# Kernel optimization log

Hardware: AMD Instinct MI355X
Metric: run time of the kernel (lower is better)

Reference implementation:

```python
import jax, jax.numpy as jnp
import numpy as np

THRESH = 0.95
SCALE = 20.0
KERNEL = 8  # feature_hw // proto_grid_size = 64 // 8
EPS = 1e-4


def _avg_pool(x, k):
    # x: [b, c, h, w] -> [b, c, h//k, w//k], non-overlapping k x k mean (AvgPool2d(k))
    b, c, h, w = x.shape
    return x.reshape(b, c, h // k, k, w // k, k).mean(axis=(3, 5))


def _safe_norm(x, eps=EPS):
    # L2-normalize along axis 1, clamping the norm at eps (matches safe_norm)
    n = jnp.sqrt(jnp.sum(x * x, axis=1, keepdims=True))
    return x / jnp.maximum(n, eps)


def setup_inputs() -> dict:
    key = jax.random.key(0)
    k1, k2, k3 = jax.random.split(key, 3)
    qry = jax.random.normal(k1, (32, 256, 64, 64), dtype=jnp.float32)
    sup_x = jax.random.normal(k2, (4, 256, 64, 64), dtype=jnp.float32)
    # binary support mask so that (sup_y > 0.95) selects the ones and pooled
    # occupancy exceeds 0.5 for ~half the grid cells -> valid prototypes exist
    sup_y = jax.random.randint(k3, (4, 1, 64, 64), 0, 2).astype(jnp.float32)
    return {"qry": qry, "sup_x": sup_x, "sup_y": sup_y}


def reference(qry, sup_x, sup_y):
    # ---- normalize query features (gridconv mode) ----
    qn = _safe_norm(qry)                                  # [B, C, H, W]

    # ---- prototype extraction (gridconv) ----
    mask_bin = (sup_y > THRESH).astype(qry.dtype)         # [bs, 1, H, W]
    feat_pooled = _avg_pool(sup_x, KERNEL)                # [bs, C, G, G]
    mask_pooled = _avg_pool(mask_bin, KERNEL)             # [bs, 1, G, G]
    valid = (mask_pooled[:, 0] > 0.5).reshape(-1)         # [P] with P = bs*G*G

    C = feat_pooled.shape[1]
    # gather all pooled locations in (image, hi, wi) order, mask out invalid ones
    protos = jnp.transpose(feat_pooled, (0, 2, 3, 1)).reshape(-1, C)  # [P, C]
    protos_n = _safe_norm(protos)                         # [P, C]

    # ---- prediction: conv2d with 1x1 prototype kernels == channel contraction ----
    dists = jnp.einsum('bchw,pc->bphw', qn, protos_n) * SCALE  # [B, P, H, W]
    vmask = valid[None, :, None, None]
    logits = jnp.where(vmask, dists, -jnp.inf)
    w = jax.nn.softmax(logits, axis=1)                    # invalid protos get 0 weight
    pred = jnp.sum(w * jnp.where(vmask, dists, 0.0), axis=1, keepdims=True)  # [B,1,H,W]

    debug_assign = jnp.argmax(logits, axis=1).astype(dists.dtype)  # [B, H, W]
    proto_grid = mask_bin                                 # (sup_y > thresh).float()
    return (pred, debug_assign, proto_grid)
```

## Files before the change

kernel.cpp:

```cpp
#include <hip/hip_runtime.h>
#include <math.h>

constexpr int BQ = 32;
constexpr int C  = 256;
constexpr int HW = 4096;
constexpr int W  = 64;
constexpr int P  = 256;
constexpr float THRESH = 0.95f;
constexpr float SCALE  = 20.0f;
constexpr float EPSF   = 1e-4f;
constexpr double EPSD  = 1e-4;
constexpr float GAP_THRESH = 2e-3f;
constexpr int MAXSUS = 65536;

constexpr int OUT_ASSIGN = BQ * HW;
constexpr int OUT_GRID   = 2 * BQ * HW;

typedef __attribute__((ext_vector_type(8))) short short8;
typedef __attribute__((ext_vector_type(4))) float floatx4;

static __device__ __forceinline__ unsigned short f2bf(float x) {
    unsigned u = __float_as_uint(x);
    u += 0x7FFFu + ((u >> 16) & 1u);
    return (unsigned short)(u >> 16);
}
static __device__ __forceinline__ float bf2f(unsigned short h) {
    return __uint_as_float(((unsigned)h) << 16);
}

#define FRAGOFF(tile, ks, h, lane) (((((tile) * 8 + (ks)) * 2 + (h)) * 64 + (lane)) * 8)

static __device__ __forceinline__ void gl_lds16(const unsigned short* gp, unsigned short* lp) {
    __builtin_amdgcn_global_load_lds(
        (const __attribute__((address_space(1))) unsigned int*)gp,
        (__attribute__((address_space(3))) unsigned int*)lp, 16, 0, 0);
}

__global__ __launch_bounds__(256)
void prep_kernel(const float* __restrict__ sup_x, const float* __restrict__ sup_y,
                 float* __restrict__ out, unsigned short* __restrict__ pB,
                 double* __restrict__ pn64, int* __restrict__ valid,
                 int* __restrict__ counter)
{
    const int p = blockIdx.x;
    const int t = threadIdx.x;
    const int s = p >> 6, gy = (p >> 3) & 7, gx = p & 7;

    const float* base = sup_x + ((size_t)(s * C + t)) * HW + (gy * 8) * W + gx * 8;
    double sum = 0.0;
#pragma unroll
    for (int r = 0; r < 8; ++r) {
        const float4 a  = *(const float4*)(base + r * W);
        const float4 bq = *(const float4*)(base + r * W + 4);
        sum += (double)a.x;  sum += (double)a.y;  sum += (double)a.z;  sum += (double)a.w;
        sum += (double)bq.x; sum += (double)bq.y; sum += (double)bq.z; sum += (double)bq.w;
    }
    const double mean = sum * (1.0 / 64.0);

    __shared__ double red[256];
    red[t] = mean * mean;
    __syncthreads();
    for (int off = 128; off > 0; off >>= 1) {
        if (t < off) red[t] += red[t + off];
        __syncthreads();
    }
    const double nrm = sqrt(red[0]);
    const double pnv = mean / fmax(nrm, EPSD);
    pn64[(size_t)p * C + t] = pnv;

    const float pnf = (float)pnv;
    const unsigned short phi = f2bf(pnf);
    const unsigned short plo = f2bf(pnf - bf2f(phi));
    const int nt = p >> 4, ks = t >> 5, lane = (((t >> 3) & 3) << 4) | (p & 15), j = t & 7;
    pB[FRAGOFF(nt, ks, 0, lane) + j] = phi;
    pB[FRAGOFF(nt, ks, 1, lane) + j] = plo;

    bool mybit = false;
    if (t < 64) {
        const int r = t >> 3, k = t & 7;
        mybit = sup_y[s * HW + (gy * 8 + r) * W + gx * 8 + k] > THRESH;
    }
    const unsigned long long bm = __ballot(mybit);
    if (t == 0) {
        valid[p] = (__popcll(bm) > 32) ? 1 : 0;
        if (p == 0) *counter = 0;
    }
    if (t < 64) {
        const int i = p * 64 + t;
        out[OUT_GRID + i] = (sup_y[i] > THRESH) ? 1.0f : 0.0f;
    }
}

__global__ __launch_bounds__(256, 2)
void dist_kernel(const float* __restrict__ qry, const unsigned short* __restrict__ pB,
                 const int* __restrict__ valid, float* __restrict__ out,
                 int* __restrict__ counter, int* __restrict__ suspects)
{
    __shared__ unsigned short ldsB[16 * 2 * 64 * 8];
    __shared__ float scale_lds[64];
    __shared__ int   validLds[P];

    const int t    = threadIdx.x;
    const int w    = t >> 6;
    const int l    = t & 63;
    const int quad = l >> 4;
    const int m    = l & 15;

    const int b    = blockIdx.x >> 6;
    const int pos0 = (blockIdx.x & 63) * 64;

    validLds[t] = valid[t];

    short8 ah[8], al[8];
    float ssq = 0.f;
    {
        const float* qp = qry + (size_t)b * C * HW + pos0 + w * 16 + m;
#pragma unroll
        for (int ks = 0; ks < 8; ++ks) {
            float v[8];
#pragma unroll
            for (int j = 0; j < 8; ++j)
                v[j] = qp[(size_t)(ks * 32 + quad * 8 + j) * HW];
            short8 h8, l8;
#pragma unroll
            for (int j = 0; j < 8; ++j) {
                ssq = fmaf(v[j], v[j], ssq);
                const unsigned short hi = f2bf(v[j]);
                h8[j] = (short)hi;
                l8[j] = (short)f2bf(v[j] - bf2f(hi));
            }
            ah[ks] = h8; al[ks] = l8;
        }
    }
    ssq += __shfl_xor(ssq, 16);
    ssq += __shfl_xor(ssq, 32);
    if (l < 16) scale_lds[w * 16 + l] = SCALE / fmaxf(sqrtf(ssq), EPSF);

    floatx4 acc[16];
#pragma unroll
    for (int nt = 0; nt < 16; ++nt) acc[nt] = (floatx4){0.f, 0.f, 0.f, 0.f};

#pragma unroll
    for (int ks = 0; ks < 8; ++ks) {
        __syncthreads();
#pragma unroll
        for (int i = 0; i < 8; ++i) {
            const int idx = w * 8 + i, nt = idx >> 1, h = idx & 1;
            gl_lds16(pB + FRAGOFF(nt, ks, h, 0) + l * 8,
                     &ldsB[(nt * 2 + h) * 512]);
        }
        __syncthreads();
#pragma unroll
        for (int nt = 0; nt < 16; ++nt) {
            const short8 bh = *(const short8*)&ldsB[((nt * 2 + 0) * 64 + l) * 8];
            const short8 bl = *(const short8*)&ldsB[((nt * 2 + 1) * 64 + l) * 8];
            acc[nt] = __builtin_amdgcn_mfma_f32_16x16x32_bf16(ah[ks], bh, acc[nt], 0, 0, 0);
            acc[nt] = __builtin_amdgcn_mfma_f32_16x16x32_bf16(ah[ks], bl, acc[nt], 0, 0, 0);
            acc[nt] = __builtin_amdgcn_mfma_f32_16x16x32_bf16(al[ks], bh, acc[nt], 0, 0, 0);
        }
    }

    int vbits = 0;
#pragma unroll
    for (int nt = 0; nt < 16; ++nt) vbits |= validLds[nt * 16 + m] << nt;

    float scr[4];
#pragma unroll
    for (int r = 0; r < 4; ++r) scr[r] = scale_lds[w * 16 + quad * 4 + r];
#pragma unroll
    for (int nt = 0; nt < 16; ++nt)
#pragma unroll
        for (int r = 0; r < 4; ++r) acc[nt][r] *= scr[r];

#pragma unroll
    for (int r = 0; r < 4; ++r) {
        float m1 = -INFINITY, m2 = -INFINITY; int id = 0x7fffffff;
#pragma unroll
        for (int nt = 0; nt < 16; ++nt) {
            if (vbits & (1 << nt)) {
                const float d = acc[nt][r];
                if (d > m1)      { m2 = m1; m1 = d; id = nt * 16 + m; }
                else if (d > m2) { m2 = d; }
            }
        }
#pragma unroll
        for (int sh = 1; sh < 16; sh <<= 1) {
            const float om1 = __shfl_xor(m1, sh);
            const float om2 = __shfl_xor(m2, sh);
            const int   oid = __shfl_xor(id, sh);
            if (om1 > m1) { m2 = fmaxf(m1, om2); m1 = om1; id = oid; }
            else { if (om1 == m1 && oid < id) id = oid; m2 = fmaxf(m2, om1); }
        }
        const int posg = b * HW + pos0 + w * 16 + quad * 4 + r;
        if (m == 0) {
            out[OUT_ASSIGN + posg] = (float)id;
            if (m1 - m2 < GAP_THRESH) {
                const int slot = atomicAdd(counter, 1);
                if (slot < MAXSUS) suspects[slot] = posg;
            }
        }
        float se = 0.f, sw = 0.f;
#pragma unroll
        for (int nt = 0; nt < 16; ++nt) {
            if (vbits & (1 << nt)) {
                const float d = acc[nt][r];
                const float e = __expf(d - m1);
                se += e; sw = fmaf(e, d, sw);
            }
        }
#pragma unroll
        for (int sh = 1; sh < 16; sh <<= 1) {
            se += __shfl_xor(se, sh);
            sw += __shfl_xor(sw, sh);
        }
        if (m == 0) out[posg] = sw / se;
    }
}

__global__ __launch_bounds__(256)
void recheck_kernel(const float* __restrict__ qry, const double* __restrict__ pn64,
                    const int* __restrict__ valid, const int* __restrict__ counter,
                    const int* __restrict__ suspects, float* __restrict__ out)
{
    __shared__ float  qsh[16][256];
    __shared__ double pd[4];
    __shared__ int    pi[4];
    const int t = threadIdx.x;
    const int w = t >> 6, l = t & 63;
    int n = *counter; if (n > MAXSUS) n = MAXSUS;
    const int nb = (n + 15) >> 4;

    for (int batch = blockIdx.x; batch < nb; batch += gridDim.x) {
        const int base = batch * 16;
        const int cnt = (n - base < 16) ? (n - base) : 16;
        for (int s = 0; s < cnt; ++s) {
            const int pos = suspects[base + s];
            qsh[s][t] = qry[(size_t)(pos >> 12) * (C * HW) + (size_t)t * HW + (pos & (HW - 1))];
        }
        __syncthreads();

        double acc[16];
#pragma unroll
        for (int s = 0; s < 16; ++s) acc[s] = 0.0;
        const double* pr = pn64 + (size_t)t * C;
#pragma unroll 4
        for (int c = 0; c < C; ++c) {
            const double pv = pr[c];
#pragma unroll
            for (int s = 0; s < 16; ++s) acc[s] = fma((double)qsh[s][c], pv, acc[s]);
        }
        const bool vl = valid[t] != 0;
        for (int s = 0; s < cnt; ++s) {
            double dv = vl ? acc[s] : -INFINITY;
            int id = t;
#pragma unroll
            for (int sh = 1; sh < 64; sh <<= 1) {
                const double od = __shfl_xor(dv, sh);
                const int    oi = __shfl_xor(id, sh);
                if (od > dv || (od == dv && oi < id)) { dv = od; id = oi; }
            }
            if (l == 0) { pd[w] = dv; pi[w] = id; }
            __syncthreads();
            if (t == 0) {
                double bd = pd[0]; int bi = pi[0];
                for (int ww = 1; ww < 4; ++ww)
                    if (pd[ww] > bd || (pd[ww] == bd && pi[ww] < bi)) { bd = pd[ww]; bi = pi[ww]; }
                out[OUT_ASSIGN + suspects[base + s]] = (float)bi;
            }
            __syncthreads();
        }
    }
}

extern "C" void kernel_launch(void* const* d_in, const int* in_sizes, int n_in,
                              void* d_out, int out_size, void* d_ws, size_t ws_size,
                              hipStream_t stream)
{
    const float* qry   = (const float*)d_in[0];
    const float* sup_x = (const float*)d_in[1];
    const float* sup_y = (const float*)d_in[2];
    float* out = (float*)d_out;
    char*  ws  = (char*)d_ws;

    unsigned short* pB       = (unsigned short*)(ws);
    double*         pn64     = (double*)(ws + 256 * 1024);
    int*            valid    = (int*)(ws + 768 * 1024);
    int*            counter  = (int*)(ws + 768 * 1024 + 1024);
    int*            suspects = (int*)(ws + 768 * 1024 + 2048);

    prep_kernel<<<dim3(P), dim3(256), 0, stream>>>(sup_x, sup_y, out, pB, pn64, valid, counter);
    dist_kernel<<<dim3(BQ * (HW / 64)), dim3(256), 0, stream>>>(qry, pB, valid, out, counter, suspects);
    recheck_kernel<<<dim3(256), dim3(256), 0, stream>>>(qry, pn64, valid, counter, suspects, out);
}
```

Measured before the change: 318.8 us.

## Stream query fragments per k-step to cut registers and raise occupancy

Instead of loading and bf16-splitting all 256 channels of the query tile into registers up front, the kernel now loads 8 floats per k-step, converts them just before the MFMAs, and prefetches the next step's values. This cuts the register footprint so launch bounds can request 4 blocks per SM instead of 2. The per-row scale is now broadcast with a shuffle rather than through LDS. The trade is that global load latency now sits inside the k-loop and is hidden only by the single-step prefetch plus the extra occupancy.

Result: faster. 292.2 us (-8.3%).

```diff
diff --git a/kernel.cpp b/kernel.cpp
--- a/kernel.cpp
+++ b/kernel.cpp
@@ -91,14 +91,13 @@
     }
 }
 
-__global__ __launch_bounds__(256, 2)
+__global__ __launch_bounds__(256, 4)
 void dist_kernel(const float* __restrict__ qry, const unsigned short* __restrict__ pB,
                  const int* __restrict__ valid, float* __restrict__ out,
                  int* __restrict__ counter, int* __restrict__ suspects)
 {
     __shared__ unsigned short ldsB[16 * 2 * 64 * 8];
-    __shared__ float scale_lds[64];
-    __shared__ int   validLds[P];
+    __shared__ int validLds[P];
 
     const int t    = threadIdx.x;
     const int w    = t >> 6;
@@ -111,35 +110,18 @@
 
     validLds[t] = valid[t];
 
-    short8 ah[8], al[8];
+    const float* qp = qry + (size_t)b * C * HW + pos0 + w * 16 + m;
+
+    floatx4 acc[16];
+#pragma unroll
+    for (int nt = 0; nt < 16; ++nt) acc[nt] = (floatx4){0.f, 0.f, 0.f, 0.f};
+
+    float vbuf[8];
+#pragma unroll
+    for (int j = 0; j < 8; ++j)
+        vbuf[j] = qp[(size_t)(quad * 8 + j) * HW];
+
     float ssq = 0.f;
-    {
-        const float* qp = qry + (size_t)b * C * HW + pos0 + w * 16 + m;
-#pragma unroll
-        for (int ks = 0; ks < 8; ++ks) {
-            float v[8];
-#pragma unroll
-            for (int j = 0; j < 8; ++j)
-                v[j] = qp[(size_t)(ks * 32 + quad * 8 + j) * HW];
-            short8 h8, l8;
-#pragma unroll
-            for (int j = 0; j < 8; ++j) {
-                ssq = fmaf(v[j], v[j], ssq);
-                const unsigned short hi = f2bf(v[j]);
-                h8[j] = (short)hi;
-                l8[j] = (short)f2bf(v[j] - bf2f(hi));
-            }
-            ah[ks] = h8; al[ks] = l8;
-        }
-    }
-    ssq += __shfl_xor(ssq, 16);
-    ssq += __shfl_xor(ssq, 32);
-    if (l < 16) scale_lds[w * 16 + l] = SCALE / fmaxf(sqrtf(ssq), EPSF);
-
-    floatx4 acc[16];
-#pragma unroll
-    for (int nt = 0; nt < 16; ++nt) acc[nt] = (floatx4){0.f, 0.f, 0.f, 0.f};
-
 #pragma unroll
     for (int ks = 0; ks < 8; ++ks) {
         __syncthreads();
@@ -149,16 +131,34 @@
             gl_lds16(pB + FRAGOFF(nt, ks, h, 0) + l * 8,
                      &ldsB[(nt * 2 + h) * 512]);
         }
+        short8 h8, l8;
+#pragma unroll
+        for (int j = 0; j < 8; ++j) {
+            const float v = vbuf[j];
+            ssq = fmaf(v, v, ssq);
+            const unsigned short hi = f2bf(v);
+            h8[j] = (short)hi;
+            l8[j] = (short)f2bf(v - bf2f(hi));
+        }
+        if (ks < 7) {
+#pragma unroll
+            for (int j = 0; j < 8; ++j)
+                vbuf[j] = qp[(size_t)((ks + 1) * 32 + quad * 8 + j) * HW];
+        }
         __syncthreads();
 #pragma unroll
         for (int nt = 0; nt < 16; ++nt) {
             const short8 bh = *(const short8*)&ldsB[((nt * 2 + 0) * 64 + l) * 8];
             const short8 bl = *(const short8*)&ldsB[((nt * 2 + 1) * 64 + l) * 8];
-            acc[nt] = __builtin_amdgcn_mfma_f32_16x16x32_bf16(ah[ks], bh, acc[nt], 0, 0, 0);
-            acc[nt] = __builtin_amdgcn_mfma_f32_16x16x32_bf16(ah[ks], bl, acc[nt], 0, 0, 0);
-            acc[nt] = __builtin_amdgcn_mfma_f32_16x16x32_bf16(al[ks], bh, acc[nt], 0, 0, 0);
-        }
-    }
+            acc[nt] = __builtin_amdgcn_mfma_f32_16x16x32_bf16(h8, bh, acc[nt], 0, 0, 0);
+            acc[nt] = __builtin_amdgcn_mfma_f32_16x16x32_bf16(h8, bl, acc[nt], 0, 0, 0);
+            acc[nt] = __builtin_amdgcn_mfma_f32_16x16x32_bf16(l8, bh, acc[nt], 0, 0, 0);
+        }
+    }
+
+    ssq += __shfl_xor(ssq, 16);
+    ssq += __shfl_xor(ssq, 32);
+    const float scalev = SCALE / fmaxf(sqrtf(ssq), EPSF);
 
     int vbits = 0;
 #pragma unroll
@@ -166,7 +166,7 @@
 
     float scr[4];
 #pragma unroll
-    for (int r = 0; r < 4; ++r) scr[r] = scale_lds[w * 16 + quad * 4 + r];
+    for (int r = 0; r < 4; ++r) scr[r] = __shfl(scalev, quad * 4 + r);
 #pragma unroll
     for (int nt = 0; nt < 16; ++nt)
 #pragma unroll
```
